# Performance work log

Measured on AMD Instinct MI355X. Metric: run time of the kernel, lower is better.

The kernel has to match this reference:

```python
import jax, jax.numpy as jnp
import numpy as np

N = 256    # number of target crystals
FB = 256   # backbone output features
D = 64     # embedding_dim
H = 4      # num_heads
DH = 128   # head_dim
L = 4      # layers
BD = 128   # expansion_size == bias_dim
AK = 100   # amd_k (edge feature dim)
EPS = 1e-5


def mish(x):
    return x * jnp.tanh(jax.nn.softplus(x))


def layernorm(x, g, b):
    m = x.mean(-1, keepdims=True)
    v = x.var(-1, keepdims=True)
    return (x - m) / jnp.sqrt(v + EPS) * g + b


def setup_inputs() -> dict:
    key = jax.random.key(0)
    ks = jax.random.split(key, 16)

    def xavier(k, shape):
        fan_in, fan_out = shape[-2], shape[-1]
        lim = float(np.sqrt(6.0 / (fan_in + fan_out)))
        return jax.random.uniform(k, shape, jnp.float32, -lim, lim)

    return dict(
        target_node_features=jax.random.normal(ks[0], (N, FB), jnp.float32),
        target_edge_features=jax.random.uniform(ks[1], (N, AK), jnp.float32),
        neighbor_target=jax.random.normal(ks[2], (N, 1), jnp.float32),
        embW=xavier(ks[3], (FB, D)), embB=jnp.zeros((D,), jnp.float32),
        boutW=xavier(ks[4], (FB, 1)), boutB=jnp.zeros((1,), jnp.float32),
        qpW=xavier(ks[5], (L, D, H * DH)), qpB=jnp.zeros((L, H * DH), jnp.float32),
        kpW=xavier(ks[6], (L, D, H * DH)), kpB=jnp.zeros((L, H * DH), jnp.float32),
        qoW=xavier(ks[7], (L, H * DH, D)), qoB=jnp.zeros((L, D), jnp.float32),
        koW=xavier(ks[8], (L, H * DH, D)), koB=jnp.zeros((L, D), jnp.float32),
        bpW=xavier(ks[9], (L, BD, H * BD)), bpB=jnp.zeros((L, H * BD), jnp.float32),
        bowW=xavier(ks[10], (L, H * BD, BD)), bowB=jnp.zeros((L, BD), jnp.float32),
        qlnG=jnp.ones((L, D), jnp.float32), qlnB=jnp.zeros((L, D), jnp.float32),
        klnG=jnp.ones((L, D), jnp.float32), klnB=jnp.zeros((L, D), jnp.float32),
    )


def reference(target_node_features, target_edge_features, neighbor_target,
              embW, embB, boutW, boutB, qpW, qpB, kpW, kpB, qoW, qoB,
              koW, koB, bpW, bpB, bowW, bowB, qlnG, qlnB, klnG, klnB):
    n = target_node_features.shape[0]
    dt = target_node_features.dtype
    eye = jnp.eye(n, dtype=dt)
    # neighbors=None path: mask = [1 - I | I], shape [N, 2N]
    mask = jnp.concatenate([1.0 - eye, eye], axis=1)

    predictions = target_node_features @ boutW + boutB          # [N,1]
    node = target_node_features @ embW + embB                   # [N,D]
    q = node
    k = jnp.concatenate([node, node], axis=0)                   # [2N,D]
    edge = jnp.concatenate([target_edge_features, target_edge_features], axis=0)  # [2N,AK]

    # cdist(target_edge, edge) with safe sqrt (zero on the exact-duplicate pairs)
    diff = target_edge_features[:, None, :] - edge[None, :, :]
    sq = jnp.sum(diff * diff, axis=-1)                           # [N,2N]
    d = jnp.where(sq > 0, jnp.sqrt(jnp.where(sq > 0, sq, 1.0)), 0.0)

    # RBFExpansion(vmin=0, vmax=cutoff=1, bins=BD): gamma = 1/mean(diff(centers))
    centers = jnp.linspace(0.0, 1.0, BD).astype(dt)
    gamma = jnp.asarray(BD - 1, dt)
    bias = jnp.exp(-gamma * (d[..., None] - centers) ** 2)       # [N,2N,BD]

    v = jnp.concatenate([neighbor_target, predictions], axis=0)  # [2N,1]

    for l in range(L):
        pq = (q @ qpW[l] + qpB[l]).reshape(n, H, DH)             # [N,H,DH]
        pk = (k @ kpW[l] + kpB[l]).reshape(2 * n, H, DH)         # [2N,H,DH]
        b = jnp.einsum('nmb,bo->nmo', bias, bpW[l]) + bpB[l]     # [N,2N,H*BD]
        diffs = jnp.linalg.norm(b.reshape(n, 2 * n, H, BD), axis=-1)  # [N,2N,H]
        logits = jnp.einsum('nhd,mhd->hnm', pq, pk) / jnp.sqrt(jnp.asarray(DH, dt))
        logits = logits + diffs.transpose(2, 0, 1)               # [H,N,2N]
        logits = jnp.where(mask[None] == 0, -9e15, logits)
        attn = jax.nn.softmax(logits, axis=-1)
        vals = jnp.einsum('hnm,mo->hno', attn, v)                # [H,N,1]
        predictions = jnp.mean(vals[:, :, 0].T, axis=-1, keepdims=True)  # [N,1]
        # permute(1,2,0).reshape: layout is (head_dim, head) interleave
        pq_flat = pq.transpose(0, 2, 1).reshape(n, H * DH)
        pk_flat = pk.transpose(0, 2, 1).reshape(2 * n, H * DH)
        q = layernorm(q + mish(pq_flat @ qoW[l] + qoB[l]), qlnG[l], qlnB[l])
        k = layernorm(k + mish(pk_flat @ koW[l] + koB[l]), klnG[l], klnB[l])
        bias = mish(jnp.einsum('nmb,bo->nmo', b, bowW[l]) + bowB[l])   # [N,2N,BD]
        v = jnp.concatenate([neighbor_target, predictions], axis=0)

    return predictions
```

## Files before the change

kernel.cpp:

```cpp
#include <hip/hip_runtime.h>

struct Params {
  const float *X, *E, *nbr;
  const float *embW, *embB, *boutW, *boutB;
  const float *qpW, *qpB, *kpW, *kpB, *qoW, *qoB, *koW, *koB;
  const float *bpW, *bpB, *bowW, *bowB;
  const float *qlnG, *qlnB, *klnG, *klnB;
  float *out;
  float *pkT;
  float *rareRow;
  float *clsDiff;
  float *rareDiff;
  unsigned *bar;
};

__device__ __forceinline__ float mishf(float x) {
  float sp = (x > 20.f) ? x : log1pf(expf(x));
  return x * tanhf(sp);
}

__device__ __forceinline__ void fma4(float4& acc, float s, const float4& v) {
  acc.x = fmaf(s, v.x, acc.x);
  acc.y = fmaf(s, v.y, acc.y);
  acc.z = fmaf(s, v.z, acc.z);
  acc.w = fmaf(s, v.w, acc.w);
}

#define LOAD8(Wp_, J0_, STRIDE_) \
  const float4 w0 = (Wp_)[(size_t)((J0_) + 0) * (STRIDE_)]; \
  const float4 w1 = (Wp_)[(size_t)((J0_) + 1) * (STRIDE_)]; \
  const float4 w2 = (Wp_)[(size_t)((J0_) + 2) * (STRIDE_)]; \
  const float4 w3 = (Wp_)[(size_t)((J0_) + 3) * (STRIDE_)]; \
  const float4 w4 = (Wp_)[(size_t)((J0_) + 4) * (STRIDE_)]; \
  const float4 w5 = (Wp_)[(size_t)((J0_) + 5) * (STRIDE_)]; \
  const float4 w6 = (Wp_)[(size_t)((J0_) + 6) * (STRIDE_)]; \
  const float4 w7 = (Wp_)[(size_t)((J0_) + 7) * (STRIDE_)];

__device__ __forceinline__ void gridBarrier(unsigned* bar, unsigned nblocks) {
  __syncthreads();
  if (threadIdx.x == 0) {
    __threadfence();
    unsigned old = atomicAdd(bar, 1u);
    if (old == nblocks - 1u) {
      atomicExch(bar + 16, 1u);
    } else {
      while (atomicAdd(bar + 16, 0u) == 0u) {
        __builtin_amdgcn_s_sleep(2);
      }
    }
    __threadfence();
  }
  __syncthreads();
}

__device__ void rare_pipe(float* row, float* drow,
                          const float* __restrict__ Wp, const float* __restrict__ Bp,
                          const float* __restrict__ Wo, const float* __restrict__ Bo,
                          float* smW, float* smS, int t) {
  const int lane = t & 63, wave = t >> 6;
  if (t < 128) smS[t] = row[t];
  __syncthreads();
  { const int o = t & 511, kh = t >> 9;
    const float* Wc = Wp + (kh * 64) * 512 + o;
    const float* rc = smS + kh * 64;
    float a = (kh == 0) ? Bp[o] : 0.f;
    #pragma unroll 8
    for (int c = 0; c < 64; ++c) a = fmaf(rc[c], Wc[c * 512], a);
    smW[t] = a; }
  __syncthreads();
  if (t < 512) smS[128 + t] = smW[t] + smW[512 + t];
  __syncthreads();
  if (wave < 4) {
    float e1 = smS[128 + wave * 128 + lane], e2 = smS[128 + wave * 128 + 64 + lane];
    float s = e1 * e1 + e2 * e2;
    #pragma unroll
    for (int sh = 32; sh; sh >>= 1) s += __shfl_xor(s, sh);
    if (lane == 0) drow[wave] = sqrtf(s);
  }
  { const int c = t & 127, ch = t >> 7;
    const float* Woc = Wo + (ch * 64) * 128 + c;
    const float* bc = smS + 128 + ch * 64;
    float a = 0.f;
    #pragma unroll 8
    for (int o2 = 0; o2 < 64; ++o2) a = fmaf(bc[o2], Woc[o2 * 128], a);
    smW[t] = a; }
  __syncthreads();
  if (t < 128) {
    float a = Bo[t];
    #pragma unroll
    for (int j = 0; j < 8; ++j) a += smW[t + 128 * j];
    row[t] = mishf(a);
  }
  __syncthreads();
}

__global__ void __launch_bounds__(1024)
__attribute__((amdgpu_waves_per_eu(4, 4)))
crakn(Params P) {
  const int b = blockIdx.x, t = threadIdx.x;
  const int lane = t & 63, wave = t >> 6;
  const int nA = 2 * b, nB = 2 * b + 1;

  __shared__ __align__(16) float smPQA[2048];
  __shared__ __align__(16) float smPQB[2048];
  __shared__ __align__(16) float smKrA[512], smKrB[512];
  __shared__ __align__(16) float smQA[64], smQB[64], smKqA[64], smKqB[64];
  __shared__ __align__(16) float smNbr[256];
  __shared__ int   smMapA[256], smMapB[256];
  __shared__ float smDiff[32];
  __shared__ __align__(16) float rowBuf[512];
  __shared__ float smPredA, smPredB;
  __shared__ int   smIA[257], smIB[257];
  __shared__ float smDA[256], smDB[256];
  __shared__ __align__(16) float4 smP4A[1024];
  __shared__ __align__(16) float4 smP4B[1024];
  __shared__ __align__(16) float smW[1024], smB2[1024], smX2[1024], smY2[1024];
  __shared__ float smH[128];
  __shared__ float smPad[512];
  if (((size_t)P.out) == 1) smPad[t & 511] = 1.f;

  if (b == 128) {
    if (t < 128) {
      float c = (float)t * (1.f / 127.f);
      rowBuf[t] = expf(-127.f * c * c);
      rowBuf[128 + t] = 0.f;
    }
    __syncthreads();
    for (int l = 0; l < 4; ++l) {
      const float* rowCur = rowBuf + (l & 1) * 256;
      float* rowNxt = rowBuf + ((l + 1) & 1) * 256;
      { const int o4 = t & 127, kc = t >> 7;
        const float4* Wf = (const float4*)(P.bpW + (size_t)l * 65536) + (size_t)(kc * 16) * 128 + o4;
        float4 az = {0.f,0.f,0.f,0.f}, ag = {0.f,0.f,0.f,0.f};
        { LOAD8(Wf, 0, 128);
          const int r = kc * 16;
          fma4(az, rowCur[r+0], w0); fma4(ag, rowCur[128+r+0], w0);
          fma4(az, rowCur[r+1], w1); fma4(ag, rowCur[128+r+1], w1);
          fma4(az, rowCur[r+2], w2); fma4(ag, rowCur[128+r+2], w2);
          fma4(az, rowCur[r+3], w3); fma4(ag, rowCur[128+r+3], w3);
          fma4(az, rowCur[r+4], w4); fma4(ag, rowCur[128+r+4], w4);
          fma4(az, rowCur[r+5], w5); fma4(ag, rowCur[128+r+5], w5);
          fma4(az, rowCur[r+6], w6); fma4(ag, rowCur[128+r+6], w6);
          fma4(az, rowCur[r+7], w7); fma4(ag, rowCur[128+r+7], w7);
        }
        { LOAD8(Wf, 8, 128);
          const int r = kc * 16 + 8;
          fma4(az, rowCur[r+0], w0); fma4(ag, rowCur[128+r+0], w0);
          fma4(az, rowCur[r+1], w1); fma4(ag, rowCur[128+r+1], w1);
          fma4(az, rowCur[r+2], w2); fma4(ag, rowCur[128+r+2], w2);
          fma4(az, rowCur[r+3], w3); fma4(ag, rowCur[128+r+3], w3);
          fma4(az, rowCur[r+4], w4); fma4(ag, rowCur[128+r+4], w4);
          fma4(az, rowCur[r+5], w5); fma4(ag, rowCur[128+r+5], w5);
          fma4(az, rowCur[r+6], w6); fma4(ag, rowCur[128+r+6], w6);
          fma4(az, rowCur[r+7], w7); fma4(ag, rowCur[128+r+7], w7);
        }
        smP4A[t] = az; smP4B[t] = ag; }
      __syncthreads();
      if (t < 512) {
        const float* pa = (const float*)smP4A;
        const float* pb = (const float*)smP4B;
        float bp = P.bpB[l * 512 + t];
        float z = bp, g2 = bp;
        #pragma unroll
        for (int kc = 0; kc < 8; ++kc) { z += pa[kc * 512 + t]; g2 += pb[kc * 512 + t]; }
        smW[t] = z; smB2[t] = g2;
      }
      __syncthreads();
      if (wave < 8) {
        const int cls = wave >> 2, h = wave & 3;
        const float* arr = cls ? smB2 : smW;
        float e1 = arr[h * 128 + lane], e2 = arr[h * 128 + 64 + lane];
        float s = e1 * e1 + e2 * e2;
        #pragma unroll
        for (int sh = 32; sh; sh >>= 1) s += __shfl_xor(s, sh);
        if (lane == 0) P.clsDiff[(l * 2 + cls) * 4 + h] = sqrtf(s);
      }
      if (l < 3) {
        { const int o4 = t & 31, kc = t >> 5;
          const float4* Wf = (const float4*)(P.bowW + (size_t)l * 65536) + (size_t)(kc * 16) * 32 + o4;
          float4 az = {0.f,0.f,0.f,0.f}, ag = {0.f,0.f,0.f,0.f};
          { LOAD8(Wf, 0, 32);
            const int r = kc * 16;
            fma4(az, smW[r+0], w0); fma4(ag, smB2[r+0], w0);
            fma4(az, smW[r+1], w1); fma4(ag, smB2[r+1], w1);
            fma4(az, smW[r+2], w2); fma4(ag, smB2[r+2], w2);
            fma4(az, smW[r+3], w3); fma4(ag, smB2[r+3], w3);
            fma4(az, smW[r+4], w4); fma4(ag, smB2[r+4], w4);
            fma4(az, smW[r+5], w5); fma4(ag, smB2[r+5], w5);
            fma4(az, smW[r+6], w6); fma4(ag, smB2[r+6], w6);
            fma4(az, smW[r+7], w7); fma4(ag, smB2[r+7], w7);
          }
          { LOAD8(Wf, 8, 32);
            const int r = kc * 16 + 8;
            fma4(az, smW[r+0], w0); fma4(ag, smB2[r+0], w0);
            fma4(az, smW[r+1], w1); fma4(ag, smB2[r+1], w1);
            fma4(az, smW[r+2], w2); fma4(ag, smB2[r+2], w2);
            fma4(az, smW[r+3], w3); fma4(ag, smB2[r+3], w3);
            fma4(az, smW[r+4], w4); fma4(ag, smB2[r+4], w4);
            fma4(az, smW[r+5], w5); fma4(ag, smB2[r+5], w5);
            fma4(az, smW[r+6], w6); fma4(ag, smB2[r+6], w6);
            fma4(az, smW[r+7], w7); fma4(ag, smB2[r+7], w7);
          }
          smP4A[t] = az; smP4B[t] = ag; }
        __syncthreads();
        if (t < 128) {
          const float* pa = (const float*)smP4A;
          const float* pb = (const float*)smP4B;
          float bo = P.bowB[l * 128 + t];
          float sz = 0.f, sg = 0.f;
          #pragma unroll
          for (int kc = 0; kc < 32; ++kc) { sz += pa[kc * 128 + t]; sg += pb[kc * 128 + t]; }
          rowNxt[t] = mishf(sz + bo);
          rowNxt[128 + t] = mishf(sg + bo);
        }
        __syncthreads();
      }
    }
  } else {
    if (t < 256) {
      smX2[t] = P.X[(size_t)nA * 256 + t];
      smY2[t] = P.X[(size_t)nB * 256 + t];
      smNbr[t] = P.nbr[t];
    }
    if (t == 0) { smIA[256] = 0; smIB[256] = 0; }
    __syncthreads();
    { const int d = t & 63, ch = t >> 6;
      const float* W = P.embW + (ch * 16) * 64 + d;
      const float* xrA = smX2 + ch * 16;
      const float* xrB = smY2 + ch * 16;
      float aA = 0.f, aB = 0.f;
      #pragma unroll
      for (int f = 0; f < 16; ++f) {
        float w = W[f * 64];
        aA = fmaf(xrA[f], w, aA);
        aB = fmaf(xrB[f], w, aB);
      }
      smW[t] = aA; smB2[t] = aB; }
    { float pp = 0.f;
      if (t < 256) pp = smX2[t] * P.boutW[t];
      else if (t < 512) pp = smY2[t - 256] * P.boutW[t - 256];
      #pragma unroll
      for (int s = 32; s; s >>= 1) pp += __shfl_xor(pp, s);
      if (t < 512 && lane == 0) smH[wave] = pp; }
    __syncthreads();
    if (t < 64) {
      float ndA = P.embB[t], ndB = P.embB[t];
      #pragma unroll
      for (int j = 0; j < 16; ++j) { ndA += smW[t + 64 * j]; ndB += smB2[t + 64 * j]; }
      smQA[t] = ndA; smKqA[t] = ndA;
      smQB[t] = ndB; smKqB[t] = ndB;
    }
    if (t == 0) {
      smPredA = smH[0] + smH[1] + smH[2] + smH[3] + P.boutB[0];
      smPredB = smH[4] + smH[5] + smH[6] + smH[7] + P.boutB[0];
    }
    if (t < 25) {
      ((float4*)rowBuf)[t]         = ((const float4*)(P.E + (size_t)nA * 100))[t];
      ((float4*)(rowBuf + 128))[t] = ((const float4*)(P.E + (size_t)nB * 100))[t];
    }
    __syncthreads();
    if (t < 512) {
      const int m = t & 255, cr = t >> 8;
      const float4* em = (const float4*)(P.E + (size_t)m * 100);
      const float4* en = (const float4*)(cr ? (rowBuf + 128) : rowBuf);
      float sq = 0.f;
      #pragma unroll 5
      for (int jj = 0; jj < 25; ++jj) {
        float4 a = en[jj], c = em[jj];
        float dx = a.x - c.x, dy = a.y - c.y, dz = a.z - c.z, dw = a.w - c.w;
        sq += dx * dx + dy * dy + dz * dz + dw * dw;
      }
      float dd = (sq > 0.f) ? sqrtf(sq) : 0.f;
      int mv;
      if (dd == 0.f) mv = -2;
      else if (dd < 1.905f) {
        int* sI = cr ? smIB : smIA;
        float* sD = cr ? smDB : smDA;
        int i = atomicAdd(&sI[256], 1);
        sI[i] = m; sD[i] = dd;
        mv = i;
      } else mv = -1;
      (cr ? smMapB : smMapA)[m] = mv;
    }
    __syncthreads();
    { int cntA = smIA[256]; if (cntA > 256) cntA = 256;
      for (int i = 0; i < cntA; ++i) if (t < 128) {
        float dd = smDA[i] - (float)t * (1.f / 127.f);
        P.rareRow[(size_t)(nA * 256 + i) * 128 + t] = expf(-127.f * dd * dd);
      }
      int cntB = smIB[256]; if (cntB > 256) cntB = 256;
      for (int i = 0; i < cntB; ++i) if (t < 128) {
        float dd = smDB[i] - (float)t * (1.f / 127.f);
        P.rareRow[(size_t)(nB * 256 + i) * 128 + t] = expf(-127.f * dd * dd);
      } }
    __syncthreads();

    for (int l = 0; l < 4; ++l) {
      { const int g = t >> 9, u = t & 511;
        const int o4 = u & 127, kc = u >> 7;
        const float4* Wf = (const float4*)((g ? P.kpW : P.qpW) + (size_t)l * 32768)
                         + (size_t)(kc * 16) * 128 + o4;
        const float* xa = g ? smKqA : smQA;
        const float* xb = g ? smKqB : smQB;
        float4 aA = {0.f,0.f,0.f,0.f}, aB = {0.f,0.f,0.f,0.f};
        { LOAD8(Wf, 0, 128);
          const int r = kc * 16;
          fma4(aA, xa[r+0], w0); fma4(aB, xb[r+0], w0);
          fma4(aA, xa[r+1], w1); fma4(aB, xb[r+1], w1);
          fma4(aA, xa[r+2], w2); fma4(aB, xb[r+2], w2);
          fma4(aA, xa[r+3], w3); fma4(aB, xb[r+3], w3);
          fma4(aA, xa[r+4], w4); fma4(aB, xb[r+4], w4);
          fma4(aA, xa[r+5], w5); fma4(aB, xb[r+5], w5);
          fma4(aA, xa[r+6], w6); fma4(aB, xb[r+6], w6);
          fma4(aA, xa[r+7], w7); fma4(aB, xb[r+7], w7);
        }
        { LOAD8(Wf, 8, 128);
          const int r = kc * 16 + 8;
          fma4(aA, xa[r+0], w0); fma4(aB, xb[r+0], w0);
          fma4(aA, xa[r+1], w1); fma4(aB, xb[r+1], w1);
          fma4(aA, xa[r+2], w2); fma4(aB, xb[r+2], w2);
          fma4(aA, xa[r+3], w3); fma4(aB, xb[r+3], w3);
          fma4(aA, xa[r+4], w4); fma4(aB, xb[r+4], w4);
          fma4(aA, xa[r+5], w5); fma4(aB, xb[r+5], w5);
          fma4(aA, xa[r+6], w6); fma4(aB, xb[r+6], w6);
          fma4(aA, xa[r+7], w7); fma4(aB, xb[r+7], w7);
        }
        smP4A[t] = aA; smP4B[t] = aB; }
      __syncthreads();
      { const int g = t >> 9, o = t & 511;
        const float* pa = (const float*)smP4A + g * 2048;
        const float* pb = (const float*)smP4B + g * 2048;
        float b0 = (g ? P.kpB : P.qpB)[l * 512 + o];
        float vA = b0 + pa[o] + pa[512 + o] + pa[1024 + o] + pa[1536 + o];
        float vB = b0 + pb[o] + pb[512 + o] + pb[1024 + o] + pb[1536 + o];
        if (g) {
          smKrA[o] = vA; smKrB[o] = vB;
          float2 st; st.x = vA; st.y = vB;
          *(float2*)(P.pkT + (size_t)l * 131072 + (size_t)o * 256 + nA) = st;
        } else { smPQA[l * 512 + o] = vA; smPQB[l * 512 + o] = vB; } }
      __syncthreads();
      if (l < 3) {
        { const int g = t >> 9, u = t & 511;
          const int o4 = u & 15, kc = u >> 4;
          const float4* Wf = (const float4*)((g ? P.koW : P.qoW) + (size_t)l * 32768)
                           + (size_t)(kc * 16) * 16 + o4;
          const float* prA = g ? smKrA : (smPQA + l * 512);
          const float* prB = g ? smKrB : (smPQB + l * 512);
          const int pb0 = kc * 4;
          float4 aA = {0.f,0.f,0.f,0.f}, aB = {0.f,0.f,0.f,0.f};
          { LOAD8(Wf, 0, 16);
            fma4(aA, prA[pb0 + 0],       w0); fma4(aB, prB[pb0 + 0],       w0);
            fma4(aA, prA[128 + pb0],     w1); fma4(aB, prB[128 + pb0],     w1);
            fma4(aA, prA[256 + pb0],     w2); fma4(aB, prB[256 + pb0],     w2);
            fma4(aA, prA[384 + pb0],     w3); fma4(aB, prB[384 + pb0],     w3);
            fma4(aA, prA[pb0 + 1],       w4); fma4(aB, prB[pb0 + 1],       w4);
            fma4(aA, prA[128 + pb0 + 1], w5); fma4(aB, prB[128 + pb0 + 1], w5);
            fma4(aA, prA[256 + pb0 + 1], w6); fma4(aB, prB[256 + pb0 + 1], w6);
            fma4(aA, prA[384 + pb0 + 1], w7); fma4(aB, prB[384 + pb0 + 1], w7);
          }
          { LOAD8(Wf, 8, 16);
            fma4(aA, prA[pb0 + 2],       w0); fma4(aB, prB[pb0 + 2],       w0);
            fma4(aA, prA[128 + pb0 + 2], w1); fma4(aB, prB[128 + pb0 + 2], w1);
            fma4(aA, prA[256 + pb0 + 2], w2); fma4(aB, prB[256 + pb0 + 2], w2);
            fma4(aA, prA[384 + pb0 + 2], w3); fma4(aB, prB[384 + pb0 + 2], w3);
            fma4(aA, prA[pb0 + 3],       w4); fma4(aB, prB[pb0 + 3],       w4);
            fma4(aA, prA[128 + pb0 + 3], w5); fma4(aB, prB[128 + pb0 + 3], w5);
            fma4(aA, prA[256 + pb0 + 3], w6); fma4(aB, prB[256 + pb0 + 3], w6);
            fma4(aA, prA[384 + pb0 + 3], w7); fma4(aB, prB[384 + pb0 + 3], w7);
          }
          smP4A[t] = aA; smP4B[t] = aB; }
        __syncthreads();
        { const int g = t >> 9, u = t & 511;
          if (u < 128) {
            const int cr = u >> 6, uu = u & 63;
            const float* src = (const float*)(cr ? smP4B : smP4A) + g * 2048;
            float acc = (g ? P.koB : P.qoB)[l * 64 + uu];
            #pragma unroll
            for (int kc = 0; kc < 32; ++kc) acc += src[kc * 64 + uu];
            float* x = g ? (cr ? smKqB : smKqA) : (cr ? smQB : smQA);
            float xv = x[uu] + mishf(acc);
            float mean = xv;
            #pragma unroll
            for (int s = 32; s; s >>= 1) mean += __shfl_xor(mean, s);
            mean *= (1.f / 64.f);
            float dv = xv - mean, var = dv * dv;
            #pragma unroll
            for (int s = 32; s; s >>= 1) var += __shfl_xor(var, s);
            var *= (1.f / 64.f);
            const float* G  = (g ? P.klnG : P.qlnG) + l * 64;
            const float* Bb = (g ? P.klnB : P.qlnB) + l * 64;
            x[uu] = dv * rsqrtf(var + 1e-5f) * G[uu] + Bb[uu];
          } }
        __syncthreads();
      }
      { int cntA = smIA[256]; if (cntA > 256) cntA = 256;
        int cntB = smIB[256]; if (cntB > 256) cntB = 256;
        if (cntA + cntB > 0) {
          __syncthreads();
          for (int i = 0; i < cntA; ++i)
            rare_pipe(P.rareRow + (size_t)(nA * 256 + i) * 128,
                      P.rareDiff + ((size_t)nA * 256 + i) * 16 + l * 4,
                      P.bpW + (size_t)l * 65536, P.bpB + l * 512,
                      P.bowW + (size_t)l * 65536, P.bowB + l * 128, smW, smX2, t);
          for (int i = 0; i < cntB; ++i)
            rare_pipe(P.rareRow + (size_t)(nB * 256 + i) * 128,
                      P.rareDiff + ((size_t)nB * 256 + i) * 16 + l * 4,
                      P.bpW + (size_t)l * 65536, P.bpB + l * 512,
                      P.bowW + (size_t)l * 65536, P.bowB + l * 128, smW, smX2, t);
        } }
    }
  }

  gridBarrier(P.bar, 129);
  if (b >= 128) return;

  if (t < 32) smDiff[t] = P.clsDiff[t];
  __syncthreads();
  {
    const int l = t >> 8, h = (t >> 6) & 3, mq = lane;
    const float* qvA = smPQA + l * 512 + h * 128;
    const float* qvB = smPQB + l * 512 + h * 128;
    const float4* pt4 = (const float4*)P.pkT + (size_t)l * 32768 + (size_t)h * 128 * 64 + mq;
    float4 dA = {0.f, 0.f, 0.f, 0.f}, dB = {0.f, 0.f, 0.f, 0.f};
    for (int jb = 0; jb < 16; ++jb) {
      const int j0 = jb * 8;
      LOAD8(pt4, j0, 64);
      fma4(dA, qvA[j0+0], w0); fma4(dB, qvB[j0+0], w0);
      fma4(dA, qvA[j0+1], w1); fma4(dB, qvB[j0+1], w1);
      fma4(dA, qvA[j0+2], w2); fma4(dB, qvB[j0+2], w2);
      fma4(dA, qvA[j0+3], w3); fma4(dB, qvB[j0+3], w3);
      fma4(dA, qvA[j0+4], w4); fma4(dB, qvB[j0+4], w4);
      fma4(dA, qvA[j0+5], w5); fma4(dB, qvB[j0+5], w5);
      fma4(dA, qvA[j0+6], w6); fma4(dB, qvB[j0+6], w6);
      fma4(dA, qvA[j0+7], w7); fma4(dB, qvB[j0+7], w7);
    }
    auto epi = [&](const float4& dot, const int* sMap, int nn, float* oH) {
      float dArr[4] = {dot.x, dot.y, dot.z, dot.w};
      float lg[4], nb[4];
      int self = -1;
      #pragma unroll
      for (int i = 0; i < 4; ++i) {
        const int m = mq * 4 + i;
        const int cls = sMap[m];
        float bd;
        if (cls >= 0) bd = P.rareDiff[((size_t)nn * 256 + cls) * 16 + l * 4 + h];
        else bd = smDiff[(l * 2 + (cls == -1 ? 1 : 0)) * 4 + h];
        lg[i] = dArr[i] * 0.08838834764831845f + bd;
        nb[i] = smNbr[m];
        if (m == nn) { self = i; nb[i] = 0.f; }
      }
      float wm = fmaxf(fmaxf(lg[0], lg[1]), fmaxf(lg[2], lg[3]));
      #pragma unroll
      for (int s = 32; s; s >>= 1) wm = fmaxf(wm, __shfl_xor(wm, s));
      float sA = 0.f, sB = 0.f, sD = 0.f;
      #pragma unroll
      for (int i = 0; i < 4; ++i) {
        float e = expf(lg[i] - wm);
        sD += e;
        sA = fmaf(e, nb[i], sA);
        if (i == self) sB = e;
      }
      #pragma unroll
      for (int s = 32; s; s >>= 1) {
        sA += __shfl_xor(sA, s); sB += __shfl_xor(sB, s); sD += __shfl_xor(sD, s);
      }
      if (lane == 0) { oH[wave] = sA; oH[16 + wave] = sB; oH[32 + wave] = sD; }
    };
    epi(dA, smMapA, nA, smH);
    epi(dB, smMapB, nB, smH + 48);
  }
  __syncthreads();
  if (t == 0 || t == 64) {
    const float* H = (t == 0) ? smH : smH + 48;
    float p = (t == 0) ? smPredA : smPredB;
    #pragma unroll
    for (int l = 0; l < 4; ++l) {
      float np = 0.f;
      #pragma unroll
      for (int h = 0; h < 4; ++h) {
        const int w = l * 4 + h;
        np += 0.25f * ((H[w] + H[16 + w] * p) / H[32 + w]);
      }
      p = np;
    }
    P.out[(t == 0) ? nA : nB] = p;
  }
}

extern "C" void kernel_launch(void* const* d_in, const int* in_sizes, int n_in,
                              void* d_out, int out_size, void* d_ws, size_t ws_size,
                              hipStream_t stream) {
  char* p = (char*)d_ws;
  auto carve = [&](size_t bytes) -> void* {
    void* r = (void*)p;
    p += (bytes + 255) & ~(size_t)255;
    return r;
  };

  Params P;
  P.X     = (const float*)d_in[0];
  P.E     = (const float*)d_in[1];
  P.nbr   = (const float*)d_in[2];
  P.embW  = (const float*)d_in[3];
  P.embB  = (const float*)d_in[4];
  P.boutW = (const float*)d_in[5];
  P.boutB = (const float*)d_in[6];
  P.qpW   = (const float*)d_in[7];
  P.qpB   = (const float*)d_in[8];
  P.kpW   = (const float*)d_in[9];
  P.kpB   = (const float*)d_in[10];
  P.qoW   = (const float*)d_in[11];
  P.qoB   = (const float*)d_in[12];
  P.koW   = (const float*)d_in[13];
  P.koB   = (const float*)d_in[14];
  P.bpW   = (const float*)d_in[15];
  P.bpB   = (const float*)d_in[16];
  P.bowW  = (const float*)d_in[17];
  P.bowB  = (const float*)d_in[18];
  P.qlnG  = (const float*)d_in[19];
  P.qlnB  = (const float*)d_in[20];
  P.klnG  = (const float*)d_in[21];
  P.klnB  = (const float*)d_in[22];
  P.out   = (float*)d_out;

  P.pkT      = (float*)carve((size_t)4 * 512 * 256 * 4);
  P.rareRow  = (float*)carve((size_t)65536 * 128 * 4);
  P.clsDiff  = (float*)carve((size_t)32 * 4);
  P.rareDiff = (float*)carve((size_t)256 * 256 * 16 * 4);
  P.bar      = (unsigned*)carve(256);

  hipMemsetAsync(P.bar, 0, 256, stream);

  hipLaunchKernelGGL(crakn, dim3(129), dim3(1024), 0, stream, P);
}
```

Before: 170.0 us.

## Keep rare-pair bias rows and diffs in shared memory instead of global scratch

Each rare neighbour pair's Gaussian-expanded bias row is now generated in shared memory and immediately pushed through all four layers of the bias pipeline. The per-layer diffs are stored in new shared arrays rather than global rareRow/rareDiff buffers. This removes large global scratch writes and reads and the interleaving of rare-pair work with the q/k layer loop. It also drops the dummy shared padding array. It adds about 32KB of LDS per block and moves the rare work before the layer loop, which may change occupancy.

New measurement: 162.8 us, median of 2. -4.2%, faster.

```diff
diff --git a/kernel.cpp b/kernel.cpp
--- a/kernel.cpp
+++ b/kernel.cpp
@@ -8,9 +8,7 @@
   const float *qlnG, *qlnB, *klnG, *klnB;
   float *out;
   float *pkT;
-  float *rareRow;
   float *clsDiff;
-  float *rareDiff;
   unsigned *bar;
 };
 
@@ -58,20 +56,19 @@
                           const float* __restrict__ Wo, const float* __restrict__ Bo,
                           float* smW, float* smS, int t) {
   const int lane = t & 63, wave = t >> 6;
-  if (t < 128) smS[t] = row[t];
   __syncthreads();
   { const int o = t & 511, kh = t >> 9;
     const float* Wc = Wp + (kh * 64) * 512 + o;
-    const float* rc = smS + kh * 64;
+    const float* rc = row + kh * 64;
     float a = (kh == 0) ? Bp[o] : 0.f;
     #pragma unroll 8
     for (int c = 0; c < 64; ++c) a = fmaf(rc[c], Wc[c * 512], a);
     smW[t] = a; }
   __syncthreads();
-  if (t < 512) smS[128 + t] = smW[t] + smW[512 + t];
+  if (t < 512) smS[t] = smW[t] + smW[512 + t];
   __syncthreads();
   if (wave < 4) {
-    float e1 = smS[128 + wave * 128 + lane], e2 = smS[128 + wave * 128 + 64 + lane];
+    float e1 = smS[wave * 128 + lane], e2 = smS[wave * 128 + 64 + lane];
     float s = e1 * e1 + e2 * e2;
     #pragma unroll
     for (int sh = 32; sh; sh >>= 1) s += __shfl_xor(s, sh);
@@ -79,7 +76,7 @@
   }
   { const int c = t & 127, ch = t >> 7;
     const float* Woc = Wo + (ch * 64) * 128 + c;
-    const float* bc = smS + 128 + ch * 64;
+    const float* bc = smS + ch * 64;
     float a = 0.f;
     #pragma unroll 8
     for (int o2 = 0; o2 < 64; ++o2) a = fmaf(bc[o2], Woc[o2 * 128], a);
@@ -108,6 +105,7 @@
   __shared__ __align__(16) float smNbr[256];
   __shared__ int   smMapA[256], smMapB[256];
   __shared__ float smDiff[32];
+  __shared__ __align__(16) float smPDA[4096], smPDB[4096];
   __shared__ __align__(16) float rowBuf[512];
   __shared__ float smPredA, smPredB;
   __shared__ int   smIA[257], smIB[257];
@@ -116,8 +114,6 @@
   __shared__ __align__(16) float4 smP4B[1024];
   __shared__ __align__(16) float smW[1024], smB2[1024], smX2[1024], smY2[1024];
   __shared__ float smH[128];
-  __shared__ float smPad[512];
-  if (((size_t)P.out) == 1) smPad[t & 511] = 1.f;
 
   if (b == 128) {
     if (t < 128) {
@@ -284,14 +280,28 @@
     }
     __syncthreads();
     { int cntA = smIA[256]; if (cntA > 256) cntA = 256;
-      for (int i = 0; i < cntA; ++i) if (t < 128) {
-        float dd = smDA[i] - (float)t * (1.f / 127.f);
-        P.rareRow[(size_t)(nA * 256 + i) * 128 + t] = expf(-127.f * dd * dd);
-      }
       int cntB = smIB[256]; if (cntB > 256) cntB = 256;
-      for (int i = 0; i < cntB; ++i) if (t < 128) {
-        float dd = smDB[i] - (float)t * (1.f / 127.f);
-        P.rareRow[(size_t)(nB * 256 + i) * 128 + t] = expf(-127.f * dd * dd);
+      if (cntA + cntB > 0) {
+        for (int i = 0; i < cntA; ++i) {
+          if (t < 128) {
+            float dd = smDA[i] - (float)t * (1.f / 127.f);
+            smY2[t] = expf(-127.f * dd * dd);
+          }
+          for (int l = 0; l < 4; ++l)
+            rare_pipe(smY2, smPDA + i * 16 + l * 4,
+                      P.bpW + (size_t)l * 65536, P.bpB + l * 512,
+                      P.bowW + (size_t)l * 65536, P.bowB + l * 128, smW, smX2, t);
+        }
+        for (int i = 0; i < cntB; ++i) {
+          if (t < 128) {
+            float dd = smDB[i] - (float)t * (1.f / 127.f);
+            smY2[t] = expf(-127.f * dd * dd);
+          }
+          for (int l = 0; l < 4; ++l)
+            rare_pipe(smY2, smPDB + i * 16 + l * 4,
+                      P.bpW + (size_t)l * 65536, P.bpB + l * 512,
+                      P.bowW + (size_t)l * 65536, P.bowB + l * 128, smW, smX2, t);
+        }
       } }
     __syncthreads();
 
@@ -393,21 +403,6 @@
           } }
         __syncthreads();
       }
-      { int cntA = smIA[256]; if (cntA > 256) cntA = 256;
-        int cntB = smIB[256]; if (cntB > 256) cntB = 256;
-        if (cntA + cntB > 0) {
-          __syncthreads();
-          for (int i = 0; i < cntA; ++i)
-            rare_pipe(P.rareRow + (size_t)(nA * 256 + i) * 128,
-                      P.rareDiff + ((size_t)nA * 256 + i) * 16 + l * 4,
-                      P.bpW + (size_t)l * 65536, P.bpB + l * 512,
-                      P.bowW + (size_t)l * 65536, P.bowB + l * 128, smW, smX2, t);
-          for (int i = 0; i < cntB; ++i)
-            rare_pipe(P.rareRow + (size_t)(nB * 256 + i) * 128,
-                      P.rareDiff + ((size_t)nB * 256 + i) * 16 + l * 4,
-                      P.bpW + (size_t)l * 65536, P.bpB + l * 512,
-                      P.bowW + (size_t)l * 65536, P.bowB + l * 128, smW, smX2, t);
-        } }
     }
   }
 
@@ -434,7 +429,7 @@
       fma4(dA, qvA[j0+6], w6); fma4(dB, qvB[j0+6], w6);
       fma4(dA, qvA[j0+7], w7); fma4(dB, qvB[j0+7], w7);
     }
-    auto epi = [&](const float4& dot, const int* sMap, int nn, float* oH) {
+    auto epi = [&](const float4& dot, const int* sMap, const float* sPD, int nn, float* oH) {
       float dArr[4] = {dot.x, dot.y, dot.z, dot.w};
       float lg[4], nb[4];
       int self = -1;
@@ -442,9 +437,9 @@
       for (int i = 0; i < 4; ++i) {
         const int m = mq * 4 + i;
         const int cls = sMap[m];
-        float bd;
-        if (cls >= 0) bd = P.rareDiff[((size_t)nn * 256 + cls) * 16 + l * 4 + h];
-        else bd = smDiff[(l * 2 + (cls == -1 ? 1 : 0)) * 4 + h];
+        const float bd = (cls == -2) ? smDiff[(l * 2 + 0) * 4 + h]
+                       : (cls == -1) ? smDiff[(l * 2 + 1) * 4 + h]
+                       : sPD[cls * 16 + l * 4 + h];
         lg[i] = dArr[i] * 0.08838834764831845f + bd;
         nb[i] = smNbr[m];
         if (m == nn) { self = i; nb[i] = 0.f; }
@@ -466,8 +461,8 @@
       }
       if (lane == 0) { oH[wave] = sA; oH[16 + wave] = sB; oH[32 + wave] = sD; }
     };
-    epi(dA, smMapA, nA, smH);
-    epi(dB, smMapB, nB, smH + 48);
+    epi(dA, smMapA, smPDA, nA, smH);
+    epi(dB, smMapB, smPDB, nB, smH + 48);
   }
   __syncthreads();
   if (t == 0 || t == 64) {
@@ -523,11 +518,9 @@
   P.klnB  = (const float*)d_in[22];
   P.out   = (float*)d_out;
 
-  P.pkT      = (float*)carve((size_t)4 * 512 * 256 * 4);
-  P.rareRow  = (float*)carve((size_t)65536 * 128 * 4);
-  P.clsDiff  = (float*)carve((size_t)32 * 4);
-  P.rareDiff = (float*)carve((size_t)256 * 256 * 16 * 4);
-  P.bar      = (unsigned*)carve(256);
+  P.pkT     = (float*)carve((size_t)4 * 512 * 256 * 4);
+  P.clsDiff = (float*)carve((size_t)32 * 4);
+  P.bar     = (unsigned*)carve(256);
 
   hipMemsetAsync(P.bar, 0, 256, stream);
 
```
